# Optimization experiments

Measured on AMD Instinct MI355X. Metric: run time of the kernel, lower is better.

The kernel has to match this reference:

```python
import jax, jax.numpy as jnp
import numpy as np

N, D, E, EDGE_DIM = 8192, 256, 262144, 1


def setup_inputs() -> dict:
    key = jax.random.key(0)
    ks = jax.random.split(key, 8)
    mag = jax.random.uniform(ks[0], (N, D), dtype=jnp.float32)
    phase = jax.random.normal(ks[1], (N, D), dtype=jnp.float32)
    edge_attr = jax.random.uniform(ks[2], (E, EDGE_DIM), dtype=jnp.float32)
    edge_index = jax.random.randint(ks[3], (2, E), 0, N, dtype=jnp.int64)
    h4 = D // 4
    w1 = jax.random.normal(ks[4], (EDGE_DIM, h4), dtype=jnp.float32) / jnp.sqrt(jnp.float32(EDGE_DIM))
    b1 = jnp.zeros((h4,), dtype=jnp.float32)
    w2 = jax.random.normal(ks[5], (h4, 1), dtype=jnp.float32) / jnp.sqrt(jnp.float32(h4))
    b2 = jnp.zeros((1,), dtype=jnp.float32)
    dist_scale = -jnp.ones((), dtype=jnp.float32)  # torch init: -1.0
    return {"mag": mag, "phase": phase, "edge_attr": edge_attr,
            "edge_index": edge_index, "w1": w1, "b1": b1, "w2": w2,
            "b2": b2, "dist_scale": dist_scale}


def reference(mag, phase, edge_attr, edge_index, w1, b1, w2, b2, dist_scale):
    # scores_ij = sum_d |z_i||z_j| cos(theta_i - theta_j) / sqrt(D)
    # cos(a-b) = cos a cos b + sin a sin b  ->  two N x D GEMMs instead of N x N x D broadcast
    d = mag.shape[-1]
    mc = mag * jnp.cos(phase)  # [N, D]
    ms = mag * jnp.sin(phase)  # [N, D]
    scores = (mc @ mc.T + ms @ ms.T) / jnp.sqrt(jnp.float32(d))  # [N, N]
    # edge bias: MLP(edge_attr) + dist_scale * distance, scattered onto (i, j) pairs
    h = jax.nn.silu(edge_attr @ w1 + b1)          # [E, D//4]
    base_bias = (h @ w2 + b2)[:, 0]               # [E]
    bias_vals = base_bias + dist_scale * edge_attr[:, 0]
    scores = scores.at[edge_index[0], edge_index[1]].add(bias_vals)
    attn = jax.nn.softmax(scores, axis=1)         # [N, N]
    new_mag = attn @ mag                          # [N, D]
    new_phase = attn @ phase                      # [N, D]
    return new_mag, new_phase
```

## Files before the change

kernel.cpp:

```cpp
#include <hip/hip_runtime.h>
#include <hip/hip_bf16.h>
#include <stdint.h>

#define N_NODES 8192
#define DD      256
#define KK      512
#define EE      262144
#define BMD     128
#define BND     32
#define NCT     64
#define CORR_CHUNK 512

typedef __attribute__((ext_vector_type(8))) short short8;
typedef __attribute__((ext_vector_type(4))) float f32x4;
typedef __attribute__((ext_vector_type(4))) unsigned int u32x4;

static __device__ __forceinline__ short f2bf(float f) {
  unsigned u = __builtin_bit_cast(unsigned, f);
  u = (u + 0x7FFFu + ((u >> 16) & 1u)) >> 16;
  return (short)u;
}
static __device__ __forceinline__ float bf2f(unsigned short s) {
  unsigned u = ((unsigned)s) << 16;
  return __builtin_bit_cast(float, u);
}

static constexpr size_t OFF_CNT  = 0;
static constexpr size_t OFF_FLAG = OFF_CNT + 32768;
static constexpr size_t OFF_L    = OFF_FLAG + 256;
static constexpr size_t OFF_OUTW = OFF_L + 32768;
static constexpr size_t MEMSET_BYTES = OFF_OUTW + 16777216;
static constexpr size_t OFF_ABF  = MEMSET_BYTES;
static constexpr size_t OFF_WT   = OFF_ABF + 8388608;
static constexpr size_t OFF_BIAS = OFF_WT + 8388608;
static constexpr size_t OFF_RP   = OFF_BIAS + 1048576;
static constexpr size_t OFF_CUR  = OFF_RP + 33024;
static constexpr size_t OFF_CCOL = OFF_CUR + 32768;
static constexpr size_t OFF_CB   = OFF_CCOL + 1048576;


__global__ void k_A(const float* __restrict__ mag, const float* __restrict__ phase,
                    short* __restrict__ Abf) {
  int g = blockIdx.x * 256 + threadIdx.x;
  int i = g >> 8, d = g & 255;
  float mg = mag[g], ph = phase[g];
  float sn, cs;
  sincosf(ph, &sn, &cs);
  Abf[(size_t)i * 512 + d]       = f2bf(mg * cs);
  Abf[(size_t)i * 512 + 256 + d] = f2bf(mg * sn);
}

__global__ void k_Wt(const float* __restrict__ mag, const float* __restrict__ phase,
                     short* __restrict__ Wt) {
  __shared__ short tt[32][520];
  int ct = blockIdx.x, tid = threadIdx.x;
  for (int h = 0; h < 2; ++h) {
    const float* src = h ? phase : mag;
#pragma unroll
    for (int m = 0; m < 32; ++m) {
      int idx = m * 256 + tid;
      int kl = idx >> 8, c = idx & 255;
      tt[kl][h * 256 + c] = f2bf(src[(size_t)(ct * 32 + kl) * 256 + c]);
    }
  }
  __syncthreads();
  short* dst = Wt + ((size_t)ct << 14);
#pragma unroll
  for (int m = 0; m < 64; ++m) {
    int idx = m * 256 + tid;
    int n = idx >> 5, kl = idx & 31;
    dst[idx] = tt[kl][n];
  }
}

__global__ void k_bias(const float* __restrict__ ea, const float* __restrict__ w1,
                       const float* __restrict__ b1, const float* __restrict__ w2,
                       const float* __restrict__ b2, const float* __restrict__ ds,
                       float* __restrict__ biasv) {
  int e = blockIdx.x * 256 + threadIdx.x;
  float x = ea[e];
  float acc = 0.f;
#pragma unroll 8
  for (int j = 0; j < 64; ++j) {
    float z = fmaf(x, w1[j], b1[j]);
    float sg = 1.f / (1.f + __expf(-z));
    acc = fmaf(z * sg, w2[j], acc);
  }
  biasv[e] = acc + b2[0] + ds[0] * x;
}

__global__ void k_detect(const unsigned* __restrict__ p, int* __restrict__ flag) {
  unsigned acc = 0;
  int idx = blockIdx.x * 256 + threadIdx.x;
  for (int t = idx; t < EE / 2; t += 64 * 256) acc |= p[2 * t + 1];
#pragma unroll
  for (int off = 32; off; off >>= 1) acc |= __shfl_xor(acc, off);
  if ((threadIdx.x & 63) == 0 && acc) atomicOr(flag, 1);
}

__device__ __forceinline__ void load_edge(const void* ei, bool is64, int e, int& i, int& j) {
  if (is64) {
    const long long* p = (const long long*)ei;
    i = (int)p[e]; j = (int)p[EE + e];
  } else {
    const int* p = (const int*)ei;
    i = p[e]; j = p[EE + e];
  }
}

__global__ void k_cnt(const void* ei, const int* __restrict__ flag, int* __restrict__ cnt) {
  int e = blockIdx.x * 256 + threadIdx.x;
  bool is64 = (*flag == 0);
  int i, j;
  load_edge(ei, is64, e, i, j);
  atomicAdd(&cnt[i], 1);
}

__global__ void k_scan(const int* __restrict__ cnt, int* __restrict__ row_ptr,
                       int* __restrict__ cursor) {
  __shared__ int part[1024];
  int tid = threadIdx.x;
  int c[8]; int s = 0;
#pragma unroll
  for (int k = 0; k < 8; ++k) { c[k] = cnt[tid * 8 + k]; s += c[k]; }
  part[tid] = s;
  __syncthreads();
  for (int off = 1; off < 1024; off <<= 1) {
    int v = part[tid];
    int add = (tid >= off) ? part[tid - off] : 0;
    __syncthreads();
    part[tid] = v + add;
    __syncthreads();
  }
  int run = part[tid] - s;
#pragma unroll
  for (int k = 0; k < 8; ++k) {
    row_ptr[tid * 8 + k] = run; cursor[tid * 8 + k] = run; run += c[k];
  }
  if (tid == 1023) row_ptr[8192] = run;
}

__global__ void k_scatter(const void* ei, const int* __restrict__ flag,
                          const float* __restrict__ biasv, int* __restrict__ cur,
                          int* __restrict__ ccol, float* __restrict__ cbias) {
  int e = blockIdx.x * 256 + threadIdx.x;
  bool is64 = (*flag == 0);
  int i, j;
  load_edge(ei, is64, e, i, j);
  int pos = atomicAdd(&cur[i], 1);
  ccol[pos] = j;
  cbias[pos] = biasv[e];
}

#define GLD16(g, l) __builtin_amdgcn_global_load_lds( \
    (const __attribute__((address_space(1))) void*)(g), \
    (__attribute__((address_space(3))) void*)(l), 16, 0, 0)

__global__ __launch_bounds__(512, 2) void k_dense(
    const short* __restrict__ Abf, const short* __restrict__ Wt,
    float* __restrict__ outw, float* __restrict__ l_arr) {
  __shared__ __align__(16) short AcB[2][BND * KK];
  __shared__ __align__(16) short WtB[2][KK * BND];
  __shared__ __align__(16) short Pl[8 * 16 * 40];

  const int tid  = threadIdx.x;
  const int lane = tid & 63;
  const int w    = tid >> 6;
  const int rlow = lane & 15;
  const int kg   = lane >> 4;

  const int bid  = blockIdx.x;
  const int sb   = (bid & 7) * 32 + (bid >> 3);
  const int part = sb >> 6;
  const int rb   = sb & 63;
  const int wrow0 = rb * BMD + w * 16;
  const int ct0   = part * NCT;

  short8 afr[16];
  {
    const short* ap = Abf + ((size_t)(wrow0 + rlow) << 9) + (kg << 3);
#pragma unroll
    for (int kb = 0; kb < 16; ++kb) afr[kb] = *(const short8*)(ap + (kb << 5));
  }
  asm volatile("s_waitcnt vmcnt(0)" ::: "memory");

#define STAGE(buf, ct) do { \
    const short* acsrc_ = Abf + ((size_t)(ct) << 14); \
    const short* wtsrc_ = Wt + ((size_t)(ct) << 14); \
    _Pragma("unroll") \
    for (int i_ = 0; i_ < 4; ++i_) { \
      int slot_ = i_ * 512 + tid; \
      int c_ = slot_ >> 6, x_ = slot_ & 63; \
      GLD16(acsrc_ + ((size_t)c_ << 9) + ((x_ ^ (c_ & 7)) << 3), \
            (char*)&AcB[buf][0] + i_ * 8192 + w * 1024); \
      GLD16(wtsrc_ + (size_t)slot_ * 8, \
            (char*)&WtB[buf][0] + i_ * 8192 + w * 1024); \
    } \
  } while (0)

  STAGE(0, ct0 + 0);
  STAGE(1, ct0 + 1);

  const f32x4 zero4 = {0.f, 0.f, 0.f, 0.f};
  f32x4 acc[32];
#pragma unroll
  for (int t = 0; t < 32; ++t) acc[t] = zero4;
  float lac[4] = {0.f, 0.f, 0.f, 0.f};
  short* plw = &Pl[w * 640];

#pragma unroll 1
  for (int ci = 0; ci < NCT; ++ci) {
    const int cur = ci & 1;
    asm volatile("s_waitcnt vmcnt(8)" ::: "memory");
    __builtin_amdgcn_s_barrier();
    __builtin_amdgcn_sched_barrier(0);

    const short* ac = &AcB[cur][0];
    f32x4 s0 = zero4, s1 = zero4;
#pragma unroll
    for (int kb = 0; kb < 16; ++kb) {
      int ch = (kb << 2) + kg;
      int sw = (ch ^ (rlow & 7)) << 3;
      short8 b0 = *(const short8*)(ac + (rlow << 9) + sw);
      short8 b1 = *(const short8*)(ac + ((16 + rlow) << 9) + sw);
      s0 = __builtin_amdgcn_mfma_f32_16x16x32_bf16(afr[kb], b0, s0, 0, 0, 0);
      s1 = __builtin_amdgcn_mfma_f32_16x16x32_bf16(afr[kb], b1, s1, 0, 0, 0);
    }

    float pr[4];
#pragma unroll
    for (int r = 0; r < 4; ++r) {
      float p0 = __expf(s0[r] * 0.0625f);
      float p1 = __expf(s1[r] * 0.0625f);
      pr[r] = p0 + p1;
      int row = (kg << 2) + r;
      plw[row * 40 + rlow]      = f2bf(p0);
      plw[row * 40 + 16 + rlow] = f2bf(p1);
    }
#pragma unroll
    for (int off = 1; off <= 8; off <<= 1) {
#pragma unroll
      for (int r = 0; r < 4; ++r) pr[r] += __shfl_xor(pr[r], off);
    }
#pragma unroll
    for (int r = 0; r < 4; ++r) lac[r] += pr[r];

    short8 pa = *(const short8*)(plw + rlow * 40 + (kg << 3));

    const short* wt = &WtB[cur][0];
#pragma unroll
    for (int t = 0; t < 32; ++t) {
      short8 wb = *(const short8*)(wt + ((t * 16 + rlow) << 5) + (kg << 3));
      acc[t] = __builtin_amdgcn_mfma_f32_16x16x32_bf16(pa, wb, acc[t], 0, 0, 0);
    }

    __builtin_amdgcn_s_barrier();
    __builtin_amdgcn_sched_barrier(0);
    STAGE(cur, ct0 + ((ci + 2) & (NCT - 1)));
  }

#pragma unroll
  for (int t = 0; t < 32; ++t) {
#pragma unroll
    for (int r = 0; r < 4; ++r) {
      int row = wrow0 + (kg << 2) + r;
      atomicAdd(&outw[((size_t)row << 9) + t * 16 + rlow], acc[t][r]);
    }
  }
  if (rlow == 0) {
#pragma unroll
    for (int r = 0; r < 4; ++r)
      atomicAdd(&l_arr[wrow0 + (kg << 2) + r], lac[r]);
  }
}
#undef STAGE
#undef GLD16

__global__ __launch_bounds__(256) void k_corr(
    const short* __restrict__ Abf, const float* __restrict__ mag,
    const float* __restrict__ phase,
    const int* __restrict__ row_ptr,
    const int* __restrict__ ccol, const float* __restrict__ cbias,
    float* __restrict__ outw, float* __restrict__ l_arr) {
  int i = blockIdx.x;
  int s = row_ptr[i], e = row_ptr[i + 1];
  if (s >= e) return;
  int tid = threadIdx.x, lane = tid & 63, w = tid >> 6;
  __shared__ float wq_s[CORR_CHUNK];

  short8 ai = *(const short8*)(Abf + ((size_t)i << 9) + (lane << 3));
  float aif[8];
#pragma unroll
  for (int u = 0; u < 8; ++u) aif[u] = bf2f((unsigned short)ai[u]);

  float accx = 0.f, accy = 0.f;
  int d = tid * 2;
  const float* wsrc = (d < 256) ? (mag + d) : (phase + (d - 256));

  for (int base = s; base < e; base += CORR_CHUNK) {
    int cl = min(e - base, CORR_CHUNK);
    for (int q = base + w; q < base + cl; q += 4) {
      int j = ccol[q];
      short8 aj = *(const short8*)(Abf + ((size_t)j << 9) + (lane << 3));
      float p = 0.f;
#pragma unroll
      for (int u = 0; u < 8; ++u) p = fmaf(aif[u], bf2f((unsigned short)aj[u]), p);
#pragma unroll
      for (int off = 32; off; off >>= 1) p += __shfl_xor(p, off);
      float bs = 0.f; int mi = 0x7FFFFFFF;
      for (int u2 = s + lane; u2 < e; u2 += 64) {
        if (ccol[u2] == j) { bs += cbias[u2]; mi = min(mi, u2); }
      }
#pragma unroll
      for (int off = 32; off; off >>= 1) {
        bs += __shfl_xor(bs, off);
        mi = min(mi, __shfl_xor(mi, off));
      }
      if (lane == 0) {
        float st = p * 0.0625f;
        wq_s[q - base] = (mi == q) ? (__expf(st + bs) - __expf(st)) : 0.f;
      }
    }
    __syncthreads();
    float lsum = 0.f;
    for (int q2 = 0; q2 < cl; ++q2) {
      float wv = wq_s[q2];
      if (wv != 0.f) {
        int j = ccol[base + q2];
        float2 t2 = *(const float2*)(wsrc + (size_t)j * 256);
        accx = fmaf(wv, t2.x, accx);
        accy = fmaf(wv, t2.y, accy);
        if (tid == 0) lsum += wv;
      }
    }
    if (tid == 0) l_arr[i] += lsum;
    __syncthreads();
  }
  outw[((size_t)i << 9) + d]     += accx;
  outw[((size_t)i << 9) + d + 1] += accy;
}

__global__ void k_norm(const float* __restrict__ o, const float* __restrict__ l_arr,
                       float* __restrict__ out) {
  int g = blockIdx.x * 256 + threadIdx.x;
  int i = g >> 9, d = g & 511;
  float v = o[g] / l_arr[i];
  size_t dst = (d < 256) ? ((size_t)i * 256 + d)
                         : ((size_t)N_NODES * 256 + (size_t)i * 256 + (d - 256));
  out[dst] = v;
}

extern "C" void kernel_launch(void* const* d_in, const int* in_sizes, int n_in,
                              void* d_out, int out_size, void* d_ws, size_t ws_size,
                              hipStream_t stream) {
  const float* mag   = (const float*)d_in[0];
  const float* phase = (const float*)d_in[1];
  const float* ea    = (const float*)d_in[2];
  const void*  ei    = d_in[3];
  const float* w1    = (const float*)d_in[4];
  const float* b1    = (const float*)d_in[5];
  const float* w2    = (const float*)d_in[6];
  const float* b2    = (const float*)d_in[7];
  const float* ds    = (const float*)d_in[8];

  char* ws = (char*)d_ws;
  int*   cnt   = (int*)(ws + OFF_CNT);
  int*   flag  = (int*)(ws + OFF_FLAG);
  float* l_arr = (float*)(ws + OFF_L);
  float* outw  = (float*)(ws + OFF_OUTW);
  short* Abf   = (short*)(ws + OFF_ABF);
  short* Wt    = (short*)(ws + OFF_WT);
  float* biasv = (float*)(ws + OFF_BIAS);
  int*   rp    = (int*)(ws + OFF_RP);
  int*   cur   = (int*)(ws + OFF_CUR);
  int*   ccol  = (int*)(ws + OFF_CCOL);
  float* cbias = (float*)(ws + OFF_CB);

  hipMemsetAsync(d_ws, 0, MEMSET_BYTES, stream);
  k_detect<<<64, 256, 0, stream>>>((const unsigned*)ei, flag);
  k_A<<<8192, 256, 0, stream>>>(mag, phase, Abf);
  k_Wt<<<256, 256, 0, stream>>>(mag, phase, Wt);
  k_bias<<<1024, 256, 0, stream>>>(ea, w1, b1, w2, b2, ds, biasv);
  k_cnt<<<1024, 256, 0, stream>>>(ei, flag, cnt);
  k_scan<<<1, 1024, 0, stream>>>(cnt, rp, cur);
  k_scatter<<<1024, 256, 0, stream>>>(ei, flag, biasv, cur, ccol, cbias);
  k_dense<<<256, 512, 0, stream>>>(Abf, Wt, outw, l_arr);
  k_corr<<<8192, 256, 0, stream>>>(Abf, mag, phase, rp, ccol, cbias, outw, l_arr);
  k_norm<<<16384, 256, 0, stream>>>(outw, l_arr, (float*)d_out);
  (void)in_sizes; (void)n_in; (void)out_size; (void)ws_size;
}
```

Baseline: 554.9 us.

## Restructure dense PV tiling, fuse bias MLP into scatter, and warp-per-row correction

The dense kernel now shares the probability tile across all waves through LDS with an extra barrier. Each wave computes a 128x64 output slab with four preloaded Wt fragments, instead of each wave covering 16 rows by all 512 dims, and setprio is added around the MFMA loops. The Wt transpose layout is changed to match the new fragment loads. The bias MLP is fused into the scatter kernel, dropping a launch and a buffer. The correction kernel now uses one wavefront per row with no block syncs, and k_detect uses more blocks. The gain is fewer LDS reads of Wt per wave, traded against an extra barrier per tile and a more complex kernel.

```diff
diff --git a/kernel.cpp b/kernel.cpp
--- a/kernel.cpp
+++ b/kernel.cpp
@@ -3,13 +3,11 @@
 #include <stdint.h>
 
 #define N_NODES 8192
-#define DD      256
 #define KK      512
 #define EE      262144
 #define BMD     128
 #define BND     32
 #define NCT     64
-#define CORR_CHUNK 512
 
 typedef __attribute__((ext_vector_type(8))) short short8;
 typedef __attribute__((ext_vector_type(4))) float f32x4;
@@ -32,8 +30,7 @@
 static constexpr size_t MEMSET_BYTES = OFF_OUTW + 16777216;
 static constexpr size_t OFF_ABF  = MEMSET_BYTES;
 static constexpr size_t OFF_WT   = OFF_ABF + 8388608;
-static constexpr size_t OFF_BIAS = OFF_WT + 8388608;
-static constexpr size_t OFF_RP   = OFF_BIAS + 1048576;
+static constexpr size_t OFF_RP   = OFF_WT + 8388608;
 static constexpr size_t OFF_CUR  = OFF_RP + 33024;
 static constexpr size_t OFF_CCOL = OFF_CUR + 32768;
 static constexpr size_t OFF_CB   = OFF_CCOL + 1048576;
@@ -68,31 +65,15 @@
 #pragma unroll
   for (int m = 0; m < 64; ++m) {
     int idx = m * 256 + tid;
-    int n = idx >> 5, kl = idx & 31;
-    dst[idx] = tt[kl][n];
-  }
-}
-
-__global__ void k_bias(const float* __restrict__ ea, const float* __restrict__ w1,
-                       const float* __restrict__ b1, const float* __restrict__ w2,
-                       const float* __restrict__ b2, const float* __restrict__ ds,
-                       float* __restrict__ biasv) {
-  int e = blockIdx.x * 256 + threadIdx.x;
-  float x = ea[e];
-  float acc = 0.f;
-#pragma unroll 8
-  for (int j = 0; j < 64; ++j) {
-    float z = fmaf(x, w1[j], b1[j]);
-    float sg = 1.f / (1.f + __expf(-z));
-    acc = fmaf(z * sg, w2[j], acc);
-  }
-  biasv[e] = acc + b2[0] + ds[0] * x;
+    int nt = idx >> 9, kgq = (idx >> 7) & 3, nl = (idx >> 3) & 15, j = idx & 7;
+    dst[idx] = tt[kgq * 8 + j][nt * 16 + nl];
+  }
 }
 
 __global__ void k_detect(const unsigned* __restrict__ p, int* __restrict__ flag) {
   unsigned acc = 0;
   int idx = blockIdx.x * 256 + threadIdx.x;
-  for (int t = idx; t < EE / 2; t += 64 * 256) acc |= p[2 * t + 1];
+  for (int t = idx; t < EE / 2; t += 256 * 256) acc |= p[2 * t + 1];
 #pragma unroll
   for (int off = 32; off; off >>= 1) acc |= __shfl_xor(acc, off);
   if ((threadIdx.x & 63) == 0 && acc) atomicOr(flag, 1);
@@ -141,15 +122,27 @@
 }
 
 __global__ void k_scatter(const void* ei, const int* __restrict__ flag,
-                          const float* __restrict__ biasv, int* __restrict__ cur,
+                          const float* __restrict__ ea,
+                          const float* __restrict__ w1, const float* __restrict__ b1,
+                          const float* __restrict__ w2, const float* __restrict__ b2,
+                          const float* __restrict__ ds,
+                          int* __restrict__ cur,
                           int* __restrict__ ccol, float* __restrict__ cbias) {
   int e = blockIdx.x * 256 + threadIdx.x;
   bool is64 = (*flag == 0);
   int i, j;
   load_edge(ei, is64, e, i, j);
+  float x = ea[e];
+  float acc = 0.f;
+#pragma unroll 8
+  for (int u = 0; u < 64; ++u) {
+    float z = fmaf(x, w1[u], b1[u]);
+    acc = fmaf(z / (1.f + __expf(-z)), w2[u], acc);
+  }
+  float bias = acc + b2[0] + ds[0] * x;
   int pos = atomicAdd(&cur[i], 1);
   ccol[pos] = j;
-  cbias[pos] = biasv[e];
+  cbias[pos] = bias;
 }
 
 #define GLD16(g, l) __builtin_amdgcn_global_load_lds( \
@@ -161,7 +154,7 @@
     float* __restrict__ outw, float* __restrict__ l_arr) {
   __shared__ __align__(16) short AcB[2][BND * KK];
   __shared__ __align__(16) short WtB[2][KK * BND];
-  __shared__ __align__(16) short Pl[8 * 16 * 40];
+  __shared__ __align__(16) short Pl[BMD * 40];
 
   const int tid  = threadIdx.x;
   const int lane = tid & 63;
@@ -173,7 +166,8 @@
   const int sb   = (bid & 7) * 32 + (bid >> 3);
   const int part = sb >> 6;
   const int rb   = sb & 63;
-  const int wrow0 = rb * BMD + w * 16;
+  const int row0 = rb * BMD;
+  const int wrow0 = row0 + w * 16;
   const int ct0   = part * NCT;
 
   short8 afr[16];
@@ -202,30 +196,33 @@
   STAGE(1, ct0 + 1);
 
   const f32x4 zero4 = {0.f, 0.f, 0.f, 0.f};
-  f32x4 acc[32];
-#pragma unroll
-  for (int t = 0; t < 32; ++t) acc[t] = zero4;
+  f32x4 acc[8][4];
+#pragma unroll
+  for (int rt = 0; rt < 8; ++rt)
+#pragma unroll
+    for (int dt = 0; dt < 4; ++dt) acc[rt][dt] = zero4;
   float lac[4] = {0.f, 0.f, 0.f, 0.f};
-  short* plw = &Pl[w * 640];
 
 #pragma unroll 1
   for (int ci = 0; ci < NCT; ++ci) {
     const int cur = ci & 1;
     asm volatile("s_waitcnt vmcnt(8)" ::: "memory");
+    __builtin_amdgcn_sched_barrier(0);
     __builtin_amdgcn_s_barrier();
     __builtin_amdgcn_sched_barrier(0);
 
     const short* ac = &AcB[cur][0];
     f32x4 s0 = zero4, s1 = zero4;
+    __builtin_amdgcn_s_setprio(1);
 #pragma unroll
     for (int kb = 0; kb < 16; ++kb) {
-      int ch = (kb << 2) + kg;
-      int sw = (ch ^ (rlow & 7)) << 3;
+      int sw = (((kb << 2) + kg) ^ (rlow & 7)) << 3;
       short8 b0 = *(const short8*)(ac + (rlow << 9) + sw);
       short8 b1 = *(const short8*)(ac + ((16 + rlow) << 9) + sw);
       s0 = __builtin_amdgcn_mfma_f32_16x16x32_bf16(afr[kb], b0, s0, 0, 0, 0);
       s1 = __builtin_amdgcn_mfma_f32_16x16x32_bf16(afr[kb], b1, s1, 0, 0, 0);
     }
+    __builtin_amdgcn_s_setprio(0);
 
     float pr[4];
 #pragma unroll
@@ -233,9 +230,9 @@
       float p0 = __expf(s0[r] * 0.0625f);
       float p1 = __expf(s1[r] * 0.0625f);
       pr[r] = p0 + p1;
-      int row = (kg << 2) + r;
-      plw[row * 40 + rlow]      = f2bf(p0);
-      plw[row * 40 + 16 + rlow] = f2bf(p1);
+      int prow = (w << 4) + (kg << 2) + r;
+      Pl[prow * 40 + rlow]      = f2bf(p0);
+      Pl[prow * 40 + 16 + rlow] = f2bf(p1);
     }
 #pragma unroll
     for (int off = 1; off <= 8; off <<= 1) {
@@ -245,14 +242,24 @@
 #pragma unroll
     for (int r = 0; r < 4; ++r) lac[r] += pr[r];
 
-    short8 pa = *(const short8*)(plw + rlow * 40 + (kg << 3));
+    asm volatile("s_waitcnt lgkmcnt(0)" ::: "memory");
+    __builtin_amdgcn_s_barrier();
+    __builtin_amdgcn_sched_barrier(0);
 
     const short* wt = &WtB[cur][0];
-#pragma unroll
-    for (int t = 0; t < 32; ++t) {
-      short8 wb = *(const short8*)(wt + ((t * 16 + rlow) << 5) + (kg << 3));
-      acc[t] = __builtin_amdgcn_mfma_f32_16x16x32_bf16(pa, wb, acc[t], 0, 0, 0);
-    }
+    short8 wtf[4];
+#pragma unroll
+    for (int dt = 0; dt < 4; ++dt)
+      wtf[dt] = *(const short8*)(wt + (((w << 2) + dt) << 9) + (kg << 7) + (rlow << 3));
+    __builtin_amdgcn_s_setprio(1);
+#pragma unroll
+    for (int rt = 0; rt < 8; ++rt) {
+      short8 pa = *(const short8*)(&Pl[((rt << 4) + rlow) * 40 + (kg << 3)]);
+#pragma unroll
+      for (int dt = 0; dt < 4; ++dt)
+        acc[rt][dt] = __builtin_amdgcn_mfma_f32_16x16x32_bf16(pa, wtf[dt], acc[rt][dt], 0, 0, 0);
+    }
+    __builtin_amdgcn_s_setprio(0);
 
     __builtin_amdgcn_s_barrier();
     __builtin_amdgcn_sched_barrier(0);
@@ -260,11 +267,15 @@
   }
 
 #pragma unroll
-  for (int t = 0; t < 32; ++t) {
-#pragma unroll
-    for (int r = 0; r < 4; ++r) {
-      int row = wrow0 + (kg << 2) + r;
-      atomicAdd(&outw[((size_t)row << 9) + t * 16 + rlow], acc[t][r]);
+  for (int rt = 0; rt < 8; ++rt) {
+#pragma unroll
+    for (int dt = 0; dt < 4; ++dt) {
+#pragma unroll
+      for (int r = 0; r < 4; ++r) {
+        int row = row0 + (rt << 4) + (kg << 2) + r;
+        int dim = (w << 6) + (dt << 4) + rlow;
+        atomicAdd(&outw[((size_t)row << 9) + dim], acc[rt][dt][r]);
+      }
     }
   }
   if (rlow == 0) {
@@ -278,66 +289,66 @@
 
 __global__ __launch_bounds__(256) void k_corr(
     const short* __restrict__ Abf, const float* __restrict__ mag,
-    const float* __restrict__ phase,
-    const int* __restrict__ row_ptr,
+    const float* __restrict__ phase, const int* __restrict__ row_ptr,
     const int* __restrict__ ccol, const float* __restrict__ cbias,
     float* __restrict__ outw, float* __restrict__ l_arr) {
-  int i = blockIdx.x;
+  int lane = threadIdx.x & 63;
+  int i = blockIdx.x * 4 + (threadIdx.x >> 6);
   int s = row_ptr[i], e = row_ptr[i + 1];
   if (s >= e) return;
-  int tid = threadIdx.x, lane = tid & 63, w = tid >> 6;
-  __shared__ float wq_s[CORR_CHUNK];
 
   short8 ai = *(const short8*)(Abf + ((size_t)i << 9) + (lane << 3));
   float aif[8];
 #pragma unroll
   for (int u = 0; u < 8; ++u) aif[u] = bf2f((unsigned short)ai[u]);
 
-  float accx = 0.f, accy = 0.f;
-  int d = tid * 2;
-  const float* wsrc = (d < 256) ? (mag + d) : (phase + (d - 256));
-
-  for (int base = s; base < e; base += CORR_CHUNK) {
-    int cl = min(e - base, CORR_CHUNK);
-    for (int q = base + w; q < base + cl; q += 4) {
-      int j = ccol[q];
-      short8 aj = *(const short8*)(Abf + ((size_t)j << 9) + (lane << 3));
-      float p = 0.f;
-#pragma unroll
-      for (int u = 0; u < 8; ++u) p = fmaf(aif[u], bf2f((unsigned short)aj[u]), p);
-#pragma unroll
-      for (int off = 32; off; off >>= 1) p += __shfl_xor(p, off);
-      float bs = 0.f; int mi = 0x7FFFFFFF;
-      for (int u2 = s + lane; u2 < e; u2 += 64) {
-        if (ccol[u2] == j) { bs += cbias[u2]; mi = min(mi, u2); }
-      }
-#pragma unroll
-      for (int off = 32; off; off >>= 1) {
-        bs += __shfl_xor(bs, off);
-        mi = min(mi, __shfl_xor(mi, off));
-      }
-      if (lane == 0) {
-        float st = p * 0.0625f;
-        wq_s[q - base] = (mi == q) ? (__expf(st + bs) - __expf(st)) : 0.f;
-      }
-    }
-    __syncthreads();
-    float lsum = 0.f;
-    for (int q2 = 0; q2 < cl; ++q2) {
-      float wv = wq_s[q2];
-      if (wv != 0.f) {
-        int j = ccol[base + q2];
-        float2 t2 = *(const float2*)(wsrc + (size_t)j * 256);
-        accx = fmaf(wv, t2.x, accx);
-        accy = fmaf(wv, t2.y, accy);
-        if (tid == 0) lsum += wv;
-      }
-    }
-    if (tid == 0) l_arr[i] += lsum;
-    __syncthreads();
-  }
-  outw[((size_t)i << 9) + d]     += accx;
-  outw[((size_t)i << 9) + d + 1] += accy;
+  int myq = s + lane;
+  bool have = myq < e;
+  int jv = have ? ccol[myq] : -1;
+  float bv = have ? cbias[myq] : 0.f;
+
+  float acc[8] = {0.f, 0.f, 0.f, 0.f, 0.f, 0.f, 0.f, 0.f};
+  float lacc = 0.f;
+  int d0 = lane << 3;
+  const float* wbase = (d0 < 256) ? (mag + d0) : (phase + (d0 - 256));
+
+  for (int q = s; q < e; ++q) {
+    int qs = q - s;
+    int j = (qs < 64) ? __shfl(jv, qs) : ccol[q];
+    short8 aj = *(const short8*)(Abf + ((size_t)j << 9) + (lane << 3));
+    f32x4 w0 = *(const f32x4*)(wbase + ((size_t)j << 8));
+    f32x4 w1 = *(const f32x4*)(wbase + ((size_t)j << 8) + 4);
+    float p = 0.f;
+#pragma unroll
+    for (int u = 0; u < 8; ++u) p = fmaf(aif[u], bf2f((unsigned short)aj[u]), p);
+    float bs = (jv == j) ? bv : 0.f;
+    int mi = (jv == j) ? myq : 0x7FFFFFFF;
+    for (int b2 = s + 64; b2 < e; b2 += 64) {
+      int q2 = b2 + lane;
+      if (q2 < e && ccol[q2] == j) { bs += cbias[q2]; mi = min(mi, q2); }
+    }
+#pragma unroll
+    for (int off = 32; off; off >>= 1) {
+      p  += __shfl_xor(p, off);
+      bs += __shfl_xor(bs, off);
+      mi  = min(mi, __shfl_xor(mi, off));
+    }
+    float st = p * 0.0625f;
+    float dw = (mi == q) ? (__expf(st + bs) - __expf(st)) : 0.f;
+    acc[0] = fmaf(dw, w0[0], acc[0]);
+    acc[1] = fmaf(dw, w0[1], acc[1]);
+    acc[2] = fmaf(dw, w0[2], acc[2]);
+    acc[3] = fmaf(dw, w0[3], acc[3]);
+    acc[4] = fmaf(dw, w1[0], acc[4]);
+    acc[5] = fmaf(dw, w1[1], acc[5]);
+    acc[6] = fmaf(dw, w1[2], acc[6]);
+    acc[7] = fmaf(dw, w1[3], acc[7]);
+    lacc += dw;
+  }
+  float* op = outw + ((size_t)i << 9) + d0;
+#pragma unroll
+  for (int u = 0; u < 8; ++u) op[u] += acc[u];
+  if (lane == 0) l_arr[i] += lacc;
 }
 
 __global__ void k_norm(const float* __restrict__ o, const float* __restrict__ l_arr,
@@ -370,22 +381,20 @@
   float* outw  = (float*)(ws + OFF_OUTW);
   short* Abf   = (short*)(ws + OFF_ABF);
   short* Wt    = (short*)(ws + OFF_WT);
-  float* biasv = (float*)(ws + OFF_BIAS);
   int*   rp    = (int*)(ws + OFF_RP);
   int*   cur   = (int*)(ws + OFF_CUR);
   int*   ccol  = (int*)(ws + OFF_CCOL);
   float* cbias = (float*)(ws + OFF_CB);
 
   hipMemsetAsync(d_ws, 0, MEMSET_BYTES, stream);
-  k_detect<<<64, 256, 0, stream>>>((const unsigned*)ei, flag);
+  k_detect<<<256, 256, 0, stream>>>((const unsigned*)ei, flag);
   k_A<<<8192, 256, 0, stream>>>(mag, phase, Abf);
   k_Wt<<<256, 256, 0, stream>>>(mag, phase, Wt);
-  k_bias<<<1024, 256, 0, stream>>>(ea, w1, b1, w2, b2, ds, biasv);
   k_cnt<<<1024, 256, 0, stream>>>(ei, flag, cnt);
   k_scan<<<1, 1024, 0, stream>>>(cnt, rp, cur);
-  k_scatter<<<1024, 256, 0, stream>>>(ei, flag, biasv, cur, ccol, cbias);
+  k_scatter<<<1024, 256, 0, stream>>>(ei, flag, ea, w1, b1, w2, b2, ds, cur, ccol, cbias);
   k_dense<<<256, 512, 0, stream>>>(Abf, Wt, outw, l_arr);
-  k_corr<<<8192, 256, 0, stream>>>(Abf, mag, phase, rp, ccol, cbias, outw, l_arr);
+  k_corr<<<2048, 256, 0, stream>>>(Abf, mag, phase, rp, ccol, cbias, outw, l_arr);
   k_norm<<<16384, 256, 0, stream>>>(outw, l_arr, (float*)d_out);
   (void)in_sizes; (void)n_in; (void)out_size; (void)ws_size;
 }
```

After: 525.4 us. 5.3% less time.
